# Kernel optimization log

Measured on AMD Instinct MI355X. Metric: run time of the kernel, lower is better.

Reference implementation:

```python
import jax, jax.numpy as jnp
import numpy as np

DIM = 1024
NUM_HEADS = 16
DH = DIM // NUM_HEADS  # 64
B, S = 4, 2048


def setup_inputs() -> dict:
    key = jax.random.key(0)
    ks = jax.random.split(key, 9)
    sc = 0.02
    x = jax.random.normal(ks[0], (B, S, DIM), dtype=jnp.float32)
    # per-head projection weights stacked: [H, DIM, DH] (input-major layout)
    Wq = jax.random.normal(ks[1], (NUM_HEADS, DIM, DH), dtype=jnp.float32) * sc
    Wk = jax.random.normal(ks[2], (NUM_HEADS, DIM, DH), dtype=jnp.float32) * sc
    Wv = jax.random.normal(ks[3], (NUM_HEADS, DIM, DH), dtype=jnp.float32) * sc
    bq = jax.random.normal(ks[4], (NUM_HEADS, DH), dtype=jnp.float32) * sc
    bk = jax.random.normal(ks[5], (NUM_HEADS, DH), dtype=jnp.float32) * sc
    bv = jax.random.normal(ks[6], (NUM_HEADS, DH), dtype=jnp.float32) * sc
    Wo = jax.random.normal(ks[7], (DIM, DIM), dtype=jnp.float32) * sc  # (in, out)
    bo = jax.random.normal(ks[8], (DIM,), dtype=jnp.float32) * sc
    return {"x": x, "Wq": Wq, "Wk": Wk, "Wv": Wv,
            "bq": bq, "bk": bk, "bv": bv, "Wo": Wo, "bo": bo}


def reference(x, Wq, Wk, Wv, bq, bk, bv, Wo, bo):
    # Per-head Linear projections, vectorized over heads: [B,H,S,DH]
    q = jnp.einsum('bsd,hde->bhse', x, Wq) + bq[None, :, None, :]
    k = jnp.einsum('bsd,hde->bhse', x, Wk) + bk[None, :, None, :]
    v = jnp.einsum('bsd,hde->bhse', x, Wv) + bv[None, :, None, :]
    # attention_matmul: Q @ K^T normalized by sqrt(dim_per_head)
    scale = 1.0 / jnp.sqrt(jnp.asarray(DH, dtype=x.dtype))
    scores = jnp.einsum('bhse,bhte->bhst', q, k) * scale  # [B,H,S,S]
    attn = jax.nn.softmax(scores, axis=-1)
    # attn_drop with p=0.0 is identity
    o = jnp.einsum('bhst,bhte->bhse', attn, v)  # [B,H,S,DH]
    # concat along last dim in head order -> [B,S,H*DH]
    o = jnp.transpose(o, (0, 2, 1, 3)).reshape(x.shape[0], x.shape[1], NUM_HEADS * DH)
    # output projection (proj_drop p=0.0 is identity)
    return o @ Wo + bo
```

## Files before the change

### kernel.cpp

```cpp
#include <hip/hip_runtime.h>
#include <stdint.h>

#define DIM 1024
#define NH 16
#define DH 64
#define BATCH 4
#define SEQ 2048
#define MROWS (BATCH*SEQ)

typedef _Float16 half8 __attribute__((ext_vector_type(8)));
typedef __fp16 fp16x2 __attribute__((ext_vector_type(2)));
typedef float f32x4 __attribute__((ext_vector_type(4)));

__device__ __forceinline__ unsigned short f2h(float f) {
    union { _Float16 h; unsigned short u; } c; c.h = (_Float16)f; return c.u;
}
__device__ __forceinline__ unsigned int pk2u(float a, float b) {
    union { fp16x2 h; unsigned int u; } c;
    c.h = __builtin_amdgcn_cvt_pkrtz(a, b);
    return c.u;
}
__device__ __forceinline__ float fexp2(float x) {
    return __builtin_amdgcn_exp2f(x);
}
__device__ __forceinline__ void gl_lds16(const unsigned short* g, unsigned short* l) {
    __builtin_amdgcn_global_load_lds(
        (__attribute__((address_space(1))) void*)(void*)g,
        (__attribute__((address_space(3))) void*)(void*)l,
        16, 0, 0);
}


__global__ void cast_x_kernel(const float* __restrict__ x,
                              unsigned short* __restrict__ xh, int n4) {
    int i = blockIdx.x * blockDim.x + threadIdx.x;
    if (i >= n4) return;
    float4 v = reinterpret_cast<const float4*>(x)[i];
    uint2 o;
    o.x = pk2u(v.x, v.y);
    o.y = pk2u(v.z, v.w);
    reinterpret_cast<uint2*>(xh)[i] = o;
}

__global__ __launch_bounds__(256) void prep_wqkv_kernel(
    const float* __restrict__ Wq, const float* __restrict__ Wk,
    const float* __restrict__ Wv, unsigned short* __restrict__ wt)
{
    __shared__ unsigned short tile[64][65];
    const int d0 = blockIdx.x * 64;
    const int h = blockIdx.y;
    const int mat = blockIdx.z;
    const float* W = (mat == 0) ? Wq : ((mat == 1) ? Wk : Wv);
    const int c = threadIdx.x & 63;
    const int rr = threadIdx.x >> 6;
#pragma unroll
    for (int p = 0; p < 16; p++) {
        int dl = p * 4 + rr;
        tile[dl][c] = f2h(W[((size_t)h * 1024 + d0 + dl) * 64 + c]);
    }
    __syncthreads();
#pragma unroll
    for (int p = 0; p < 16; p++) {
        int el = p * 4 + rr;
        wt[(((size_t)(mat * NH + h) * 64) + el) * DIM + d0 + c] = tile[c][el];
    }
}

__global__ __launch_bounds__(256) void prep_wo_kernel(
    const float* __restrict__ Wo, unsigned short* __restrict__ wot)
{
    __shared__ unsigned short tile[64][65];
    const int d0 = blockIdx.x * 64;
    const int o0 = blockIdx.y * 64;
    const int c = threadIdx.x & 63;
    const int rr = threadIdx.x >> 6;
#pragma unroll
    for (int p = 0; p < 16; p++) {
        int dl = p * 4 + rr;
        tile[dl][c] = f2h(Wo[(size_t)(d0 + dl) * DIM + o0 + c]);
    }
    __syncthreads();
#pragma unroll
    for (int p = 0; p < 16; p++) {
        int ol = p * 4 + rr;
        wot[(size_t)(o0 + ol) * DIM + d0 + c] = tile[c][ol];
    }
}

__global__ __launch_bounds__(256) void transpose_v_kernel(
    const unsigned short* __restrict__ Vb, unsigned short* __restrict__ Vt)
{
    __shared__ unsigned short tile[64][65];
    const int s0 = blockIdx.x * 64;
    const size_t bh = (size_t)blockIdx.z * NH + blockIdx.y;
    const int c = threadIdx.x & 63;
    const int rr = threadIdx.x >> 6;
    const unsigned short* src = Vb + bh * SEQ * DH;
    unsigned short* dst = Vt + bh * DH * SEQ;
#pragma unroll
    for (int p = 0; p < 16; p++) {
        int sl = p * 4 + rr;
        tile[sl][c] = src[(size_t)(s0 + sl) * DH + c];
    }
    __syncthreads();
#pragma unroll
    for (int p = 0; p < 16; p++) {
        int dr = p * 4 + rr;
        dst[(size_t)dr * SEQ + s0 + c] = tile[c][dr];
    }
}

__global__ __launch_bounds__(256) void qkv_gemm_kernel(
    const unsigned short* __restrict__ xh,
    const unsigned short* __restrict__ wt,
    const float* __restrict__ bq, const float* __restrict__ bk,
    const float* __restrict__ bv,
    unsigned short* __restrict__ Qb,
    unsigned short* __restrict__ Kb,
    unsigned short* __restrict__ Vb)
{
    const int rowblk = blockIdx.x;
    const int hpair = blockIdx.y;
    const int mat = blockIdx.z;
    const int wave = threadIdx.x >> 6;
    const int lane = threadIdx.x & 63;
    const int quad = lane >> 4;
    const int lr = lane & 15;
    const int mhalf = wave & 1;
    const int nhalf = wave >> 1;

    __shared__ __align__(16) unsigned short Ab[2][128 * 32];
    __shared__ __align__(16) unsigned short Bt[2][128 * 32];

    const unsigned short* Asrc = xh + (size_t)rowblk * 128 * DIM;
    const unsigned short* Bsrc = wt + (size_t)(mat * NH + hpair * 2) * DH * DIM;

    const int srow = lane >> 2;
    const int scs = lane & 3;

    f32x4 acc[4][4];
#pragma unroll
    for (int mt = 0; mt < 4; mt++)
#pragma unroll
        for (int nt = 0; nt < 4; nt++) acc[mt][nt] = (f32x4){0.f, 0.f, 0.f, 0.f};

    auto stage = [&](int k0, int sel) {
#pragma unroll
        for (int jj = 0; jj < 2; jj++) {
            const int j = wave * 2 + jj;
            const int r = j * 16 + srow;
            const int cg = scs ^ ((r >> 1) & 3);
            gl_lds16(Asrc + (size_t)r * DIM + k0 + cg * 8, &Ab[sel][j * 512]);
            gl_lds16(Bsrc + (size_t)r * DIM + k0 + cg * 8, &Bt[sel][j * 512]);
        }
    };

    stage(0, 0);
    __syncthreads();

    for (int i = 0; i < DIM / 32; i++) {
        const int sel = i & 1;
        if (i + 1 < DIM / 32) stage((i + 1) * 32, sel ^ 1);

        half8 af[4], bf[4];
#pragma unroll
        for (int mt = 0; mt < 4; mt++) {
            const int row = mhalf * 64 + mt * 16 + lr;
            const int slot = quad ^ ((row >> 1) & 3);
            af[mt] = *reinterpret_cast<const half8*>(&Ab[sel][row * 32 + slot * 8]);
        }
#pragma unroll
        for (int nt = 0; nt < 4; nt++) {
            const int row = nhalf * 64 + nt * 16 + lr;
            const int slot = quad ^ ((row >> 1) & 3);
            bf[nt] = *reinterpret_cast<const half8*>(&Bt[sel][row * 32 + slot * 8]);
        }
#pragma unroll
        for (int mt = 0; mt < 4; mt++)
#pragma unroll
            for (int nt = 0; nt < 4; nt++)
                acc[mt][nt] = __builtin_amdgcn_mfma_f32_16x16x32_f16(
                    af[mt], bf[nt], acc[mt][nt], 0, 0, 0);
        __syncthreads();
    }

    const float* bias = (mat == 0) ? bq : ((mat == 1) ? bk : bv);
    const float scale = (mat == 0) ? 0.1803368801111601f : 1.0f;
    unsigned short* outp = (mat == 0) ? Qb : ((mat == 1) ? Kb : Vb);
    const int rowBase = rowblk * 128 + mhalf * 64;
    const int bb = rowBase / SEQ;
    const int sBase = rowBase % SEQ;

#pragma unroll
    for (int mt = 0; mt < 4; mt++) {
        const int s0 = sBase + mt * 16 + quad * 4;
#pragma unroll
        for (int nt = 0; nt < 4; nt++) {
            const int e = nhalf * 64 + nt * 16 + lr;
            const int head = hpair * 2 + (e >> 6);
            const int n = e & 63;
            const float bvl = bias[head * DH + n];
            const size_t base = (size_t)(bb * NH + head) * SEQ * DH;
#pragma unroll
            for (int r = 0; r < 4; r++) {
                outp[base + (size_t)(s0 + r) * DH + n] = f2h((acc[mt][nt][r] + bvl) * scale);
            }
        }
    }
}

__global__ __launch_bounds__(256) void attn_kernel(
    const unsigned short* __restrict__ Qb,
    const unsigned short* __restrict__ Kb,
    const unsigned short* __restrict__ Vt,
    unsigned short* __restrict__ Ob)
{
    const int h = blockIdx.y;
    const int bb = blockIdx.z;
    const int wave = threadIdx.x >> 6;
    const int lane = threadIdx.x & 63;
    const int quad = lane >> 4;
    const int lr = lane & 15;
    const int qBase = blockIdx.x * 128 + wave * 32;

    const size_t bh = (size_t)(bb * NH + h);
    const unsigned short* Qh = Qb + bh * SEQ * DH;
    const unsigned short* Kh = Kb + bh * SEQ * DH;
    const unsigned short* Vh = Vt + bh * DH * SEQ;

    __shared__ __align__(16) unsigned short Kbuf[2][64 * 64];
    __shared__ __align__(16) unsigned short Vbuf[2][64 * 64];
    __shared__ __align__(16) unsigned short Pall[4][32 * 72];
    unsigned short* Pw = Pall[wave];

    const int srow = lane >> 3;
    const int scs = lane & 7;
    const int cg = scs ^ srow;
    int koff[2], voff[2];
#pragma unroll
    for (int jj = 0; jj < 2; jj++) {
        const int r = wave * 16 + jj * 8 + srow;
        koff[jj] = r * DH + cg * 8;
        voff[jj] = r * SEQ + cg * 8;
    }

    auto stage = [&](int kt, int sel) {
        gl_lds16(Kh + (size_t)kt * DH + koff[0], &Kbuf[sel][wave * 1024]);
        gl_lds16(Kh + (size_t)kt * DH + koff[1], &Kbuf[sel][wave * 1024 + 512]);
        gl_lds16(Vh + kt + voff[0], &Vbuf[sel][wave * 1024]);
        gl_lds16(Vh + kt + voff[1], &Vbuf[sel][wave * 1024 + 512]);
    };

    half8 qf[2][2];
#pragma unroll
    for (int mt = 0; mt < 2; mt++)
#pragma unroll
        for (int kc = 0; kc < 2; kc++)
            qf[mt][kc] = *reinterpret_cast<const half8*>(
                Qh + (size_t)(qBase + mt * 16 + lr) * DH + kc * 32 + quad * 8);

    const f32x4 zf = {0.f, 0.f, 0.f, 0.f};
    f32x4 o[4][2];
    float lsum[2] = {0.f, 0.f};
#pragma unroll
    for (int t = 0; t < 4; t++)
#pragma unroll
        for (int mt = 0; mt < 2; mt++) o[t][mt] = zf;

    auto compute = [&](int sel) {
        f32x4 sacc[4][2];
#pragma unroll
        for (int kc = 0; kc < 2; kc++) {
            half8 kf[4];
#pragma unroll
            for (int t = 0; t < 4; t++) {
                const int row = t * 16 + lr;
                const int slot = (kc * 4 + quad) ^ (row & 7);
                kf[t] = *reinterpret_cast<const half8*>(&Kbuf[sel][row * 64 + slot * 8]);
            }
#pragma unroll
            for (int t = 0; t < 4; t++)
#pragma unroll
                for (int mt = 0; mt < 2; mt++)
                    sacc[t][mt] = __builtin_amdgcn_mfma_f32_16x16x32_f16(
                        kf[t], qf[mt][kc], kc ? sacc[t][mt] : zf, 0, 0, 0);
        }

#pragma unroll
        for (int t = 0; t < 4; t++)
#pragma unroll
            for (int mt = 0; mt < 2; mt++) {
                float p0 = fexp2(sacc[t][mt][0]);
                float p1 = fexp2(sacc[t][mt][1]);
                float p2 = fexp2(sacc[t][mt][2]);
                float p3 = fexp2(sacc[t][mt][3]);
                lsum[mt] += (p0 + p1) + (p2 + p3);
                uint2 w;
                w.x = pk2u(p0, p1);
                w.y = pk2u(p2, p3);
                *reinterpret_cast<uint2*>(&Pw[(mt * 16 + lr) * 72 + t * 16 + quad * 4]) = w;
            }

#pragma unroll
        for (int kc = 0; kc < 2; kc++) {
            half8 pf[2];
#pragma unroll
            for (int mt = 0; mt < 2; mt++)
                pf[mt] = *reinterpret_cast<const half8*>(
                    &Pw[(mt * 16 + lr) * 72 + kc * 32 + quad * 8]);
            half8 vf[4];
#pragma unroll
            for (int t = 0; t < 4; t++) {
                const int row = t * 16 + lr;
                const int slot = (kc * 4 + quad) ^ (row & 7);
                vf[t] = *reinterpret_cast<const half8*>(&Vbuf[sel][row * 64 + slot * 8]);
            }
#pragma unroll
            for (int t = 0; t < 4; t++)
#pragma unroll
                for (int mt = 0; mt < 2; mt++)
                    o[t][mt] = __builtin_amdgcn_mfma_f32_16x16x32_f16(
                        vf[t], pf[mt], o[t][mt], 0, 0, 0);
        }
    };

    stage(0, 0);
    __syncthreads();

    for (int i = 0; i < SEQ / 64; i += 2) {
        stage((i + 1) * 64, 1);
        compute(0);
        __syncthreads();
        if (i + 2 < SEQ / 64) stage((i + 2) * 64, 0);
        compute(1);
        __syncthreads();
    }

    float inv[2];
#pragma unroll
    for (int mt = 0; mt < 2; mt++) {
        float l = lsum[mt];
        l += __shfl_xor(l, 16);
        l += __shfl_xor(l, 32);
        inv[mt] = 1.f / l;
    }
#pragma unroll
    for (int t = 0; t < 4; t++)
#pragma unroll
        for (int mt = 0; mt < 2; mt++) {
            uint2 pkd;
            pkd.x = pk2u(o[t][mt][0] * inv[mt], o[t][mt][1] * inv[mt]);
            pkd.y = pk2u(o[t][mt][2] * inv[mt], o[t][mt][3] * inv[mt]);
            const int q = qBase + mt * 16 + lr;
            *reinterpret_cast<uint2*>(
                Ob + ((size_t)(bb * SEQ + q)) * DIM + h * DH + t * 16 + quad * 4) = pkd;
        }
}

__global__ __launch_bounds__(256) void out_proj_kernel(
    const unsigned short* __restrict__ Ob,
    const unsigned short* __restrict__ wot,
    const float* __restrict__ bo,
    float* __restrict__ out)
{
    const int rowblk = blockIdx.x;
    const int colblk = blockIdx.y;
    const int wave = threadIdx.x >> 6;
    const int lane = threadIdx.x & 63;
    const int quad = lane >> 4;
    const int lr = lane & 15;
    const int mhalf = wave & 1;
    const int nhalf = wave >> 1;

    __shared__ __align__(16) unsigned short Ab[2][128 * 32];
    __shared__ __align__(16) unsigned short Bt[2][128 * 32];

    const unsigned short* Asrc = Ob + (size_t)rowblk * 128 * DIM;
    const unsigned short* Bsrc = wot + (size_t)colblk * 128 * DIM;

    const int srow = lane >> 2;
    const int scs = lane & 3;

    f32x4 acc[4][4];
#pragma unroll
    for (int mt = 0; mt < 4; mt++)
#pragma unroll
        for (int nt = 0; nt < 4; nt++) acc[mt][nt] = (f32x4){0.f, 0.f, 0.f, 0.f};

    auto stage = [&](int k0, int sel) {
#pragma unroll
        for (int jj = 0; jj < 2; jj++) {
            const int j = wave * 2 + jj;
            const int r = j * 16 + srow;
            const int cg = scs ^ ((r >> 1) & 3);
            gl_lds16(Asrc + (size_t)r * DIM + k0 + cg * 8, &Ab[sel][j * 512]);
            gl_lds16(Bsrc + (size_t)r * DIM + k0 + cg * 8, &Bt[sel][j * 512]);
        }
    };

    stage(0, 0);
    __syncthreads();

    for (int i = 0; i < DIM / 32; i++) {
        const int sel = i & 1;
        if (i + 1 < DIM / 32) stage((i + 1) * 32, sel ^ 1);

        half8 af[4], bf[4];
#pragma unroll
        for (int mt = 0; mt < 4; mt++) {
            const int row = mhalf * 64 + mt * 16 + lr;
            const int slot = quad ^ ((row >> 1) & 3);
            af[mt] = *reinterpret_cast<const half8*>(&Ab[sel][row * 32 + slot * 8]);
        }
#pragma unroll
        for (int nt = 0; nt < 4; nt++) {
            const int row = nhalf * 64 + nt * 16 + lr;
            const int slot = quad ^ ((row >> 1) & 3);
            bf[nt] = *reinterpret_cast<const half8*>(&Bt[sel][row * 32 + slot * 8]);
        }
#pragma unroll
        for (int mt = 0; mt < 4; mt++)
#pragma unroll
            for (int nt = 0; nt < 4; nt++)
                acc[mt][nt] = __builtin_amdgcn_mfma_f32_16x16x32_f16(
                    af[mt], bf[nt], acc[mt][nt], 0, 0, 0);
        __syncthreads();
    }

    const int rowBase = rowblk * 128 + mhalf * 64;
    const int colBase = colblk * 128 + nhalf * 64;
#pragma unroll
    for (int mt = 0; mt < 4; mt++) {
#pragma unroll
        for (int nt = 0; nt < 4; nt++) {
            const int col = colBase + nt * 16 + lr;
            const float bias = bo[col];
#pragma unroll
            for (int r = 0; r < 4; r++) {
                int row = rowBase + mt * 16 + quad * 4 + r;
                out[(size_t)row * DIM + col] = acc[mt][nt][r] + bias;
            }
        }
    }
}


extern "C" void kernel_launch(void* const* d_in, const int* in_sizes, int n_in,
                              void* d_out, int out_size, void* d_ws, size_t ws_size,
                              hipStream_t stream) {
    const float* x  = (const float*)d_in[0];
    const float* Wq = (const float*)d_in[1];
    const float* Wk = (const float*)d_in[2];
    const float* Wv = (const float*)d_in[3];
    const float* bq = (const float*)d_in[4];
    const float* bk = (const float*)d_in[5];
    const float* bv = (const float*)d_in[6];
    const float* Wo = (const float*)d_in[7];
    const float* bo = (const float*)d_in[8];
    float* out = (float*)d_out;

    unsigned short* xh  = (unsigned short*)d_ws;
    unsigned short* wt  = xh  + (size_t)MROWS * DIM;
    unsigned short* wot = wt  + (size_t)3 * NH * DH * DIM;
    unsigned short* Qb  = wot + (size_t)DIM * DIM;
    unsigned short* Kb  = Qb  + (size_t)BATCH * NH * SEQ * DH;
    unsigned short* Vb  = Kb  + (size_t)BATCH * NH * SEQ * DH;
    unsigned short* Vt  = Vb  + (size_t)BATCH * NH * SEQ * DH;
    unsigned short* Ob  = Vt  + (size_t)BATCH * NH * SEQ * DH;

    {
        int n4 = MROWS * DIM / 4;
        cast_x_kernel<<<(n4 + 255) / 256, 256, 0, stream>>>(x, xh, n4);
    }
    prep_wqkv_kernel<<<dim3(16, NH, 3), 256, 0, stream>>>(Wq, Wk, Wv, wt);
    prep_wo_kernel<<<dim3(16, 16), 256, 0, stream>>>(Wo, wot);
    qkv_gemm_kernel<<<dim3(64, 8, 3), 256, 0, stream>>>(xh, wt, bq, bk, bv, Qb, Kb, Vb);
    transpose_v_kernel<<<dim3(SEQ / 64, NH, BATCH), 256, 0, stream>>>(Vb, Vt);
    attn_kernel<<<dim3(SEQ / 128, NH, BATCH), 256, 0, stream>>>(Qb, Kb, Vt, Ob);
    out_proj_kernel<<<dim3(64, 8), 256, 0, stream>>>(Ob, wot, bo, out);
}
```

Baseline: 313.0 us.

## Use 32x32x16 MFMA in attention with register-resident P via cross-lane shuffles

Rewrites the attention inner loop around 32x32x16 MFMA tiles, with each wave now handling 64 query rows instead of 32. The S^T accumulator layout is repacked into the B operand of the PV MFMA through lane-xor-32 shuffles, so the per-wave LDS round trip for P goes away. The grid is reordered so heads/batches vary fastest, and launch bounds request 2 blocks per CU. This halves the K/V LDS reads per query and removes P staging, at the cost of higher register pressure from the 16-wide accumulators. It also halves the block count, which may hurt occupancy.

After: 523.3 us. +67.2%, slower.

```diff
diff --git a/kernel.cpp b/kernel.cpp
--- a/kernel.cpp
+++ b/kernel.cpp
@@ -11,6 +11,7 @@
 typedef _Float16 half8 __attribute__((ext_vector_type(8)));
 typedef __fp16 fp16x2 __attribute__((ext_vector_type(2)));
 typedef float f32x4 __attribute__((ext_vector_type(4)));
+typedef float f32x16 __attribute__((ext_vector_type(16)));
 
 __device__ __forceinline__ unsigned short f2h(float f) {
     union { _Float16 h; unsigned short u; } c; c.h = (_Float16)f; return c.u;
@@ -28,6 +29,11 @@
         (__attribute__((address_space(1))) void*)(void*)g,
         (__attribute__((address_space(3))) void*)(void*)l,
         16, 0, 0);
+}
+__device__ __forceinline__ half8 u4h8(unsigned a, unsigned b, unsigned c, unsigned d) {
+    union { unsigned u[4]; half8 h; } x;
+    x.u[0] = a; x.u[1] = b; x.u[2] = c; x.u[3] = d;
+    return x.h;
 }
 
 
@@ -209,19 +215,20 @@
     }
 }
 
-__global__ __launch_bounds__(256) void attn_kernel(
+__global__ __launch_bounds__(256, 2) void attn_kernel(
     const unsigned short* __restrict__ Qb,
     const unsigned short* __restrict__ Kb,
     const unsigned short* __restrict__ Vt,
     unsigned short* __restrict__ Ob)
 {
-    const int h = blockIdx.y;
-    const int bb = blockIdx.z;
+    const int hb = blockIdx.x;
+    const int h = hb & 15;
+    const int bb = hb >> 4;
     const int wave = threadIdx.x >> 6;
     const int lane = threadIdx.x & 63;
-    const int quad = lane >> 4;
-    const int lr = lane & 15;
-    const int qBase = blockIdx.x * 128 + wave * 32;
+    const int l31 = lane & 31;
+    const int hh = lane >> 5;
+    const int qBase = blockIdx.y * 256 + wave * 64;
 
     const size_t bh = (size_t)(bb * NH + h);
     const unsigned short* Qh = Qb + bh * SEQ * DH;
@@ -230,8 +237,6 @@
 
     __shared__ __align__(16) unsigned short Kbuf[2][64 * 64];
     __shared__ __align__(16) unsigned short Vbuf[2][64 * 64];
-    __shared__ __align__(16) unsigned short Pall[4][32 * 72];
-    unsigned short* Pw = Pall[wave];
 
     const int srow = lane >> 3;
     const int scs = lane & 7;
@@ -243,7 +248,6 @@
         koff[jj] = r * DH + cg * 8;
         voff[jj] = r * SEQ + cg * 8;
     }
-
     auto stage = [&](int kt, int sel) {
         gl_lds16(Kh + (size_t)kt * DH + koff[0], &Kbuf[sel][wave * 1024]);
         gl_lds16(Kh + (size_t)kt * DH + koff[1], &Kbuf[sel][wave * 1024 + 512]);
@@ -251,82 +255,97 @@
         gl_lds16(Vh + kt + voff[1], &Vbuf[sel][wave * 1024 + 512]);
     };
 
-    half8 qf[2][2];
-#pragma unroll
-    for (int mt = 0; mt < 2; mt++)
-#pragma unroll
-        for (int kc = 0; kc < 2; kc++)
-            qf[mt][kc] = *reinterpret_cast<const half8*>(
-                Qh + (size_t)(qBase + mt * 16 + lr) * DH + kc * 32 + quad * 8);
-
-    const f32x4 zf = {0.f, 0.f, 0.f, 0.f};
-    f32x4 o[4][2];
+    half8 qf[2][4];
+#pragma unroll
+    for (int qt = 0; qt < 2; qt++)
+#pragma unroll
+        for (int kc = 0; kc < 4; kc++)
+            qf[qt][kc] = *reinterpret_cast<const half8*>(
+                Qh + (size_t)(qBase + qt * 32 + l31) * DH + kc * 16 + hh * 8);
+
+    f32x16 o[2][2];
+#pragma unroll
+    for (int ds = 0; ds < 2; ds++)
+#pragma unroll
+        for (int qt = 0; qt < 2; qt++)
+#pragma unroll
+            for (int r = 0; r < 16; r++) o[ds][qt][r] = 0.f;
     float lsum[2] = {0.f, 0.f};
-#pragma unroll
-    for (int t = 0; t < 4; t++)
-#pragma unroll
-        for (int mt = 0; mt < 2; mt++) o[t][mt] = zf;
+
+    const f32x16 zf16 = {0.f};
 
     auto compute = [&](int sel) {
-        f32x4 sacc[4][2];
-#pragma unroll
-        for (int kc = 0; kc < 2; kc++) {
-            half8 kf[4];
-#pragma unroll
-            for (int t = 0; t < 4; t++) {
-                const int row = t * 16 + lr;
-                const int slot = (kc * 4 + quad) ^ (row & 7);
-                kf[t] = *reinterpret_cast<const half8*>(&Kbuf[sel][row * 64 + slot * 8]);
+        half8 kf[2][4];
+#pragma unroll
+        for (int ks = 0; ks < 2; ks++)
+#pragma unroll
+            for (int kc = 0; kc < 4; kc++) {
+                const int row = ks * 32 + l31;
+                const int slot = (kc * 2 + hh) ^ (row & 7);
+                kf[ks][kc] = *reinterpret_cast<const half8*>(&Kbuf[sel][row * 64 + slot * 8]);
             }
-#pragma unroll
-            for (int t = 0; t < 4; t++)
-#pragma unroll
-                for (int mt = 0; mt < 2; mt++)
-                    sacc[t][mt] = __builtin_amdgcn_mfma_f32_16x16x32_f16(
-                        kf[t], qf[mt][kc], kc ? sacc[t][mt] : zf, 0, 0, 0);
-        }
-
-#pragma unroll
-        for (int t = 0; t < 4; t++)
-#pragma unroll
-            for (int mt = 0; mt < 2; mt++) {
-                float p0 = fexp2(sacc[t][mt][0]);
-                float p1 = fexp2(sacc[t][mt][1]);
-                float p2 = fexp2(sacc[t][mt][2]);
-                float p3 = fexp2(sacc[t][mt][3]);
-                lsum[mt] += (p0 + p1) + (p2 + p3);
-                uint2 w;
-                w.x = pk2u(p0, p1);
-                w.y = pk2u(p2, p3);
-                *reinterpret_cast<uint2*>(&Pw[(mt * 16 + lr) * 72 + t * 16 + quad * 4]) = w;
+        half8 vf[2][4];
+#pragma unroll
+        for (int ds = 0; ds < 2; ds++)
+#pragma unroll
+            for (int c = 0; c < 4; c++) {
+                const int row = ds * 32 + l31;
+                const int slot = (c * 2 + hh) ^ (row & 7);
+                vf[ds][c] = *reinterpret_cast<const half8*>(&Vbuf[sel][row * 64 + slot * 8]);
             }
 
-#pragma unroll
-        for (int kc = 0; kc < 2; kc++) {
-            half8 pf[2];
-#pragma unroll
-            for (int mt = 0; mt < 2; mt++)
-                pf[mt] = *reinterpret_cast<const half8*>(
-                    &Pw[(mt * 16 + lr) * 72 + kc * 32 + quad * 8]);
-            half8 vf[4];
-#pragma unroll
-            for (int t = 0; t < 4; t++) {
-                const int row = t * 16 + lr;
-                const int slot = (kc * 4 + quad) ^ (row & 7);
-                vf[t] = *reinterpret_cast<const half8*>(&Vbuf[sel][row * 64 + slot * 8]);
+        unsigned BB[2][4][4];
+#pragma unroll
+        for (int qt = 0; qt < 2; qt++) {
+            f32x16 sacc[2];
+#pragma unroll
+            for (int kc = 0; kc < 4; kc++)
+#pragma unroll
+                for (int ks = 0; ks < 2; ks++)
+                    sacc[ks] = __builtin_amdgcn_mfma_f32_32x32x16_f16(
+                        kf[ks][kc], qf[qt][kc], kc ? sacc[ks] : zf16, 0, 0, 0);
+
+            unsigned P2[2][8];
+#pragma unroll
+            for (int ks = 0; ks < 2; ks++)
+#pragma unroll
+                for (int j = 0; j < 8; j++) {
+                    float p0 = fexp2(sacc[ks][2 * j]);
+                    float p1 = fexp2(sacc[ks][2 * j + 1]);
+                    lsum[qt] += p0 + p1;
+                    P2[ks][j] = pk2u(p0, p1);
+                }
+
+#pragma unroll
+            for (int c = 0; c < 4; c++) {
+                const int ks = c >> 1, cl = c & 1;
+                unsigned own0 = hh ? P2[ks][4 * cl + 2] : P2[ks][4 * cl + 0];
+                unsigned own1 = hh ? P2[ks][4 * cl + 3] : P2[ks][4 * cl + 1];
+                unsigned oth0 = hh ? P2[ks][4 * cl + 0] : P2[ks][4 * cl + 2];
+                unsigned oth1 = hh ? P2[ks][4 * cl + 1] : P2[ks][4 * cl + 3];
+                unsigned xa = __shfl_xor((int)oth0, 32);
+                unsigned xb = __shfl_xor((int)oth1, 32);
+                BB[qt][c][0] = hh ? xa : own0;
+                BB[qt][c][1] = hh ? xb : own1;
+                BB[qt][c][2] = hh ? own0 : xa;
+                BB[qt][c][3] = hh ? own1 : xb;
             }
-#pragma unroll
-            for (int t = 0; t < 4; t++)
-#pragma unroll
-                for (int mt = 0; mt < 2; mt++)
-                    o[t][mt] = __builtin_amdgcn_mfma_f32_16x16x32_f16(
-                        vf[t], pf[mt], o[t][mt], 0, 0, 0);
-        }
+        }
+
+#pragma unroll
+        for (int c = 0; c < 4; c++)
+#pragma unroll
+            for (int ds = 0; ds < 2; ds++)
+#pragma unroll
+                for (int qt = 0; qt < 2; qt++)
+                    o[ds][qt] = __builtin_amdgcn_mfma_f32_32x32x16_f16(
+                        vf[ds][c],
+                        u4h8(BB[qt][c][0], BB[qt][c][1], BB[qt][c][2], BB[qt][c][3]),
+                        o[ds][qt], 0, 0, 0);
     };
 
     stage(0, 0);
     __syncthreads();
-
     for (int i = 0; i < SEQ / 64; i += 2) {
         stage((i + 1) * 64, 1);
         compute(0);
@@ -338,22 +357,23 @@
 
     float inv[2];
 #pragma unroll
-    for (int mt = 0; mt < 2; mt++) {
-        float l = lsum[mt];
-        l += __shfl_xor(l, 16);
-        l += __shfl_xor(l, 32);
-        inv[mt] = 1.f / l;
-    }
-#pragma unroll
-    for (int t = 0; t < 4; t++)
-#pragma unroll
-        for (int mt = 0; mt < 2; mt++) {
-            uint2 pkd;
-            pkd.x = pk2u(o[t][mt][0] * inv[mt], o[t][mt][1] * inv[mt]);
-            pkd.y = pk2u(o[t][mt][2] * inv[mt], o[t][mt][3] * inv[mt]);
-            const int q = qBase + mt * 16 + lr;
-            *reinterpret_cast<uint2*>(
-                Ob + ((size_t)(bb * SEQ + q)) * DIM + h * DH + t * 16 + quad * 4) = pkd;
+    for (int qt = 0; qt < 2; qt++) {
+        float l = lsum[qt] + __shfl_xor(lsum[qt], 32);
+        inv[qt] = 1.f / l;
+    }
+#pragma unroll
+    for (int ds = 0; ds < 2; ds++)
+#pragma unroll
+        for (int qt = 0; qt < 2; qt++) {
+            const int q = qBase + qt * 32 + l31;
+            unsigned short* obq = Ob + ((size_t)(bb * SEQ + q)) * DIM + h * DH;
+#pragma unroll
+            for (int r = 0; r < 4; r++) {
+                uint2 pkd;
+                pkd.x = pk2u(o[ds][qt][4 * r] * inv[qt], o[ds][qt][4 * r + 1] * inv[qt]);
+                pkd.y = pk2u(o[ds][qt][4 * r + 2] * inv[qt], o[ds][qt][4 * r + 3] * inv[qt]);
+                *reinterpret_cast<uint2*>(obq + ds * 32 + 8 * r + 4 * hh) = pkd;
+            }
         }
 }
 
@@ -476,6 +496,6 @@
     prep_wo_kernel<<<dim3(16, 16), 256, 0, stream>>>(Wo, wot);
     qkv_gemm_kernel<<<dim3(64, 8, 3), 256, 0, stream>>>(xh, wt, bq, bk, bv, Qb, Kb, Vb);
     transpose_v_kernel<<<dim3(SEQ / 64, NH, BATCH), 256, 0, stream>>>(Vb, Vt);
-    attn_kernel<<<dim3(SEQ / 128, NH, BATCH), 256, 0, stream>>>(Qb, Kb, Vt, Ob);
+    attn_kernel<<<dim3(64, SEQ / 256), 256, 0, stream>>>(Qb, Kb, Vt, Ob);
     out_proj_kernel<<<dim3(64, 8), 256, 0, stream>>>(Ob, wot, bo, out);
 }
```
